# Optimization experiments

Hardware: AMD Instinct MI355X
Metric: run time of the kernel (lower is better)

Reference implementation:

```python
import math
import jax, jax.numpy as jnp
import numpy as np

N, L, H, E, K = 4, 768, 8, 64, 1  # batch, seq (L==S), heads, feat, num_sines


def setup_inputs() -> dict:
    key = jax.random.key(0)
    ks = jax.random.split(key, 8)
    queries = jax.random.normal(ks[0], (N, L, H, E), jnp.float32)
    keys = jax.random.normal(ks[1], (N, L, H, E), jnp.float32)
    values = jax.random.normal(ks[2], (N, L, H, E), jnp.float32)
    attn_mask_add = jnp.zeros((L, L), jnp.float32)
    key_lengths_add = jnp.zeros((N, L), jnp.float32)
    freqs = jax.random.normal(ks[3], (H, E, K), jnp.float32) - 4.0  # init shift
    offsets = jax.random.normal(ks[4], (H, E, K), jnp.float32)
    gains = jax.random.normal(ks[5], (H, E, K), jnp.float32)
    # gains.data /= sqrt(||gains||_{-1}) / 2
    gains = gains / (jnp.sqrt(jnp.linalg.norm(gains, axis=-1, keepdims=True)) / 2.0)
    gate = jax.random.normal(ks[6], (H, E), jnp.float32)
    return dict(queries=queries, keys=keys, values=values,
                attn_mask_add=attn_mask_add, key_lengths_add=key_lengths_add,
                freqs=freqs, offsets=offsets, gains=gains, gate=gate)


def reference(queries, keys, values, attn_mask_add, key_lengths_add,
              freqs, offsets, gains, gate):
    n, l, h, e = queries.shape
    softmax_temp = 1.0 / math.sqrt(e)
    positions = jnp.arange(l, dtype=queries.dtype)  # (L,)
    f = jax.nn.sigmoid(freqs)[None] / 2.0  # (1,H,E,K)
    phases_q = 2.0 * math.pi * f * positions[:, None, None, None] + offsets[None]
    phases_k = 2.0 * math.pi * f * positions[:, None, None, None]
    # interleave cos/sin along last dim -> (L,H,E,2K)
    omega_q = jnp.stack([jnp.cos(phases_q), jnp.sin(phases_q)], axis=-1).reshape(l, h, e, 2 * f.shape[-1])
    omega_k = jnp.stack([jnp.cos(phases_k), jnp.sin(phases_k)], axis=-1).reshape(l, h, e, 2 * f.shape[-1])
    g = jax.nn.softplus(gains)
    g2 = jnp.stack([g, g], axis=-1).reshape(h, e, 2 * f.shape[-1])  # (H,E,2K)
    # positional kernel P: (L,S,H,E)
    P = jnp.einsum('lhdk,hdk,shdk->lshd', omega_q, g2 ** 2, omega_k)
    P = (1.0 - gate) * P + gate  # gated
    QK = jnp.einsum('nlhd,lshd,nshd->nhls', queries, P, keys)
    QK = QK + attn_mask_add[None, None] + key_lengths_add[:, None, None, :]
    A = jax.nn.softmax(softmax_temp * QK, axis=-1)
    V = jnp.einsum('nhls,nshd->nlhd', A, values)
    return V
```

## Files before the change

kernel.cpp:

```cpp
#include <hip/hip_runtime.h>
#include <math.h>
#include <stdint.h>

#define NB 4
#define LQ 768
#define NH 8
#define NE 64
#define ND 192
#define TEMP 0.125f

typedef _Float16 f16;
typedef __attribute__((ext_vector_type(8))) _Float16 f16x8;
typedef __attribute__((ext_vector_type(4))) float f32x4;

__device__ __forceinline__ void stage16(f16* lds_base, const f16* g, int lane) {
#if __has_builtin(__builtin_amdgcn_global_load_lds)
    __builtin_amdgcn_global_load_lds(
        (const __attribute__((address_space(1))) uint32_t*)g,
        (__attribute__((address_space(3))) uint32_t*)lds_base, 16, 0, 0);
#else
    *(uint4*)((char*)lds_base + lane * 16) = *(const uint4*)g;
#endif
}

template <int CTRL>
__device__ __forceinline__ float dppf(float x) {
    union { float f; int i; } u, r;
    u.f = x;
    r.i = __builtin_amdgcn_update_dpp(u.i, u.i, CTRL, 0xF, 0xF, false);
    return r.f;
}
__device__ __forceinline__ float red16_max(float x) {
    x = fmaxf(x, dppf<0xB1>(x));
    x = fmaxf(x, dppf<0x4E>(x));
    x = fmaxf(x, dppf<0x141>(x));
    x = fmaxf(x, dppf<0x140>(x));
    return x;
}
__device__ __forceinline__ float red16_sum(float x) {
    x += dppf<0xB1>(x);
    x += dppf<0x4E>(x);
    x += dppf<0x141>(x);
    x += dppf<0x140>(x);
    return x;
}

__global__ __launch_bounds__(256) void sinattn_prep(
    const float* __restrict__ Q, const float* __restrict__ K,
    const float* __restrict__ freqs, const float* __restrict__ offsets,
    const float* __restrict__ gains, const float* __restrict__ gate,
    f16* __restrict__ Qf, f16* __restrict__ Kf)
{
    int idx = blockIdx.x * 256 + threadIdx.x;
    int eg = idx & 7, e0 = eg << 3;
    int h  = (idx >> 3) & 7;
    int t  = idx >> 6;
    int l  = t % LQ;
    int n  = t / LQ;
    int nh = (n << 3) | h;
    int he = (h << 6) | e0;

    const float* qp = Q + (size_t)idx * 8;
    const float* kp = K + (size_t)idx * 8;
    float4 q0 = *(const float4*)qp, q1 = *(const float4*)(qp + 4);
    float4 k0 = *(const float4*)kp, k1 = *(const float4*)(kp + 4);
    float qv[8] = {q0.x,q0.y,q0.z,q0.w, q1.x,q1.y,q1.z,q1.w};
    float kv[8] = {k0.x,k0.y,k0.z,k0.w, k1.x,k1.y,k1.z,k1.w};

    float4 fA = *(const float4*)(freqs   + he), fB = *(const float4*)(freqs   + he + 4);
    float4 oA = *(const float4*)(offsets + he), oB = *(const float4*)(offsets + he + 4);
    float4 gA = *(const float4*)(gains   + he), gB = *(const float4*)(gains   + he + 4);
    float4 tA = *(const float4*)(gate    + he), tB = *(const float4*)(gate    + he + 4);
    float fv[8] = {fA.x,fA.y,fA.z,fA.w, fB.x,fB.y,fB.z,fB.w};
    float ov[8] = {oA.x,oA.y,oA.z,oA.w, oB.x,oB.y,oB.z,oB.w};
    float gv[8] = {gA.x,gA.y,gA.z,gA.w, gB.x,gB.y,gB.z,gB.w};
    float tv[8] = {tA.x,tA.y,tA.z,tA.w, tB.x,tB.y,tB.z,tB.w};

    f16x8 oq0, oq1, oq2, ok0, ok1, ok2;
    float lf = (float)l;
    #pragma unroll
    for (int j = 0; j < 8; ++j) {
        float f  = 0.5f / (1.0f + __expf(-fv[j]));
        float gn = gv[j];
        float sp = (gn > 15.0f) ? gn : __logf(1.0f + __expf(gn));
        float gt = tv[j];
        float a  = (1.0f - gt) * sp * sp;
        float fh = __uint_as_float(__float_as_uint(f) & 0xFFFFF000u);
        float fl = f - fh;
        float t0 = lf * fh;
        float tr = t0 - floorf(t0);
        tr = __builtin_fmaf(lf, fl, tr);
        float pk = 6.28318530717958647f * tr;
        float pq = pk + ov[j];
        float sq = __sinf(pq), cq = __cosf(pq);
        float sk = __sinf(pk), ck = __cosf(pk);
        oq0[j] = (f16)(qv[j] * a * cq);
        oq1[j] = (f16)(qv[j] * a * sq);
        oq2[j] = (f16)(qv[j] * gt);
        ok0[j] = (f16)(kv[j] * ck);
        ok1[j] = (f16)(kv[j] * sk);
        ok2[j] = (f16)(kv[j]);
    }
    size_t base = ((size_t)nh * LQ + l) * ND + e0;
    *(f16x8*)(Qf + base)            = oq0;
    *(f16x8*)(Qf + base + NE)       = oq1;
    *(f16x8*)(Qf + base + 2 * NE)   = oq2;
    *(f16x8*)(Kf + base)            = ok0;
    *(f16x8*)(Kf + base + NE)       = ok1;
    *(f16x8*)(Kf + base + 2 * NE)   = ok2;
}

__global__ __launch_bounds__(256) void sinattn_vt(
    const float* __restrict__ V, f16* __restrict__ Vt)
{
    __shared__ f16 tile[64][72];
    int b = blockIdx.x;
    int st = b % 12, nh = b / 12;
    int n = nh >> 3, h = nh & 7;
    int s0 = st * 64;
    int tid = threadIdx.x;

    int sl = tid >> 2, e0 = (tid & 3) << 4;
    const float4* vp = (const float4*)(V + ((size_t)(n * LQ + s0 + sl) * NH + h) * NE + e0);
    float4 a0 = vp[0], a1 = vp[1], a2 = vp[2], a3 = vp[3];
    float vv[16] = { a0.x,a0.y,a0.z,a0.w, a1.x,a1.y,a1.z,a1.w,
                     a2.x,a2.y,a2.z,a2.w, a3.x,a3.y,a3.z,a3.w };
    #pragma unroll
    for (int j = 0; j < 16; ++j) tile[e0 + j][sl] = (f16)vv[j];
    __syncthreads();

    int er = tid >> 2, sc = tid & 3;
    f16* op = Vt + ((size_t)nh * NE + er) * LQ + s0 + sc * 16;
    *(uint4*)op       = *(const uint4*)&tile[er][sc * 16];
    *(uint4*)(op + 8) = *(const uint4*)&tile[er][sc * 16 + 8];
}

__global__ __launch_bounds__(128, 2) void sinattn_flash(
    const f16* __restrict__ Qf, const f16* __restrict__ Kf, const f16* __restrict__ Vt,
    const float* __restrict__ mask, const float* __restrict__ keylen,
    float* __restrict__ out)
{
    __shared__ __attribute__((aligned(16))) f16 sK[2][64 * 24 * 8];
    __shared__ __attribute__((aligned(16))) f16 sV[2][64 * 8 * 8];
    __shared__ __attribute__((aligned(16))) f16 sP[2][32 * 72];

    int tid  = threadIdx.x;
    int wv   = tid >> 6;
    int lane = tid & 63;
    int grp  = lane >> 4;
    int r16  = lane & 15;
    int swz  = r16 & 7;

    int bid = blockIdx.x;
    int nh  = bid & 31;
    int lt  = bid >> 5;
    int n   = nh >> 3;
    int l0  = lt * 64;

    f16x8 qf[2][6];
    #pragma unroll
    for (int ti = 0; ti < 2; ++ti) {
        size_t rbase = ((size_t)nh * LQ + l0 + wv * 32 + ti * 16 + r16) * ND + grp * 8;
        #pragma unroll
        for (int d0 = 0; d0 < 6; ++d0)
            qf[ti][d0] = *(const f16x8*)(Qf + rbase + d0 * 32);
    }

    int goffK[12], goffV[4];
    #pragma unroll
    for (int i = 0; i < 12; ++i) {
        int p = i * 128 + tid;
        int r = p / 24, c = p - r * 24;
        int cl = (c & ~7) | ((c & 7) ^ (r & 7));
        goffK[i] = r * ND + cl * 8;
    }
    #pragma unroll
    for (int i = 0; i < 4; ++i) {
        int p = i * 128 + tid;
        int r = p >> 3, c = p & 7;
        goffV[i] = r * LQ + (c ^ (r & 7)) * 8;
    }
    const f16* Kb = Kf + (size_t)nh * LQ * ND;
    const f16* Vb = Vt + (size_t)nh * NE * LQ;

    {
        #pragma unroll
        for (int i = 0; i < 12; ++i)
            stage16(&sK[0][(i * 128 + wv * 64) * 8], Kb + goffK[i], lane);
        #pragma unroll
        for (int i = 0; i < 4; ++i)
            stage16(&sV[0][(i * 128 + wv * 64) * 8], Vb + goffV[i], lane);
    }

    float m_i[2][4], l_i[2][4];
    f32x4 O[2][4];
    #pragma unroll
    for (int ti = 0; ti < 2; ++ti)
        #pragma unroll
        for (int rr = 0; rr < 4; ++rr) { m_i[ti][rr] = -INFINITY; l_i[ti][rr] = 0.f; }
    #pragma unroll
    for (int ti = 0; ti < 2; ++ti)
        #pragma unroll
        for (int tt = 0; tt < 4; ++tt)
            #pragma unroll
            for (int rr = 0; rr < 4; ++rr) O[ti][tt][rr] = 0.f;

    for (int c = 0; c < 12; ++c) {
        int cur = c & 1;
        int s0  = c * 64;
        __syncthreads();

        if (c < 11) {
            const f16* kg = Kb + (s0 + 64) * ND;
            const f16* vg = Vb + (s0 + 64);
            #pragma unroll
            for (int i = 0; i < 12; ++i)
                stage16(&sK[cur ^ 1][(i * 128 + wv * 64) * 8], kg + goffK[i], lane);
            #pragma unroll
            for (int i = 0; i < 4; ++i)
                stage16(&sV[cur ^ 1][(i * 128 + wv * 64) * 8], vg + goffV[i], lane);
        }

        float klv[4], mreg[2][4][4];
        #pragma unroll
        for (int j = 0; j < 4; ++j) klv[j] = keylen[n * LQ + s0 + j * 16 + r16];
        #pragma unroll
        for (int ti = 0; ti < 2; ++ti)
            #pragma unroll
            for (int rr = 0; rr < 4; ++rr) {
                int lrow = l0 + wv * 32 + ti * 16 + grp * 4 + rr;
                #pragma unroll
                for (int j = 0; j < 4; ++j)
                    mreg[ti][rr][j] = mask[lrow * LQ + s0 + j * 16 + r16];
            }

        f32x4 st[2][4];
        #pragma unroll
        for (int ti = 0; ti < 2; ++ti)
            #pragma unroll
            for (int j = 0; j < 4; ++j)
                #pragma unroll
                for (int rr = 0; rr < 4; ++rr) st[ti][j][rr] = 0.f;
        #pragma unroll
        for (int d0 = 0; d0 < 6; ++d0) {
            #pragma unroll
            for (int j = 0; j < 4; ++j) {
                int cc = d0 * 4 + grp;
                int cl = (cc & ~7) | ((cc & 7) ^ swz);
                f16x8 bf = *(const f16x8*)&sK[cur][((j * 16 + r16) * 24 + cl) * 8];
                st[0][j] = __builtin_amdgcn_mfma_f32_16x16x32_f16(qf[0][d0], bf, st[0][j], 0, 0, 0);
                st[1][j] = __builtin_amdgcn_mfma_f32_16x16x32_f16(qf[1][d0], bf, st[1][j], 0, 0, 0);
            }
        }

        #pragma unroll
        for (int ti = 0; ti < 2; ++ti) {
            #pragma unroll
            for (int rr = 0; rr < 4; ++rr) {
                float lg[4];
                float mx = -INFINITY;
                #pragma unroll
                for (int j = 0; j < 4; ++j) {
                    lg[j] = TEMP * (st[ti][j][rr] + mreg[ti][rr][j] + klv[j]);
                    mx = fmaxf(mx, lg[j]);
                }
                mx = red16_max(mx);
                float mnew  = fmaxf(m_i[ti][rr], mx);
                float alpha = __expf(m_i[ti][rr] - mnew);
                float rs = 0.f;
                #pragma unroll
                for (int j = 0; j < 4; ++j) {
                    float p = __expf(lg[j] - mnew);
                    rs += p;
                    sP[wv][(ti * 16 + grp * 4 + rr) * 72 + j * 16 + r16] = (f16)p;
                }
                rs = red16_sum(rs);
                l_i[ti][rr] = l_i[ti][rr] * alpha + rs;
                m_i[ti][rr] = mnew;
                #pragma unroll
                for (int tt = 0; tt < 4; ++tt) O[ti][tt][rr] *= alpha;
            }
        }

        #pragma unroll
        for (int kk = 0; kk < 2; ++kk) {
            f16x8 pa0 = *(const f16x8*)&sP[wv][(r16) * 72 + kk * 32 + grp * 8];
            f16x8 pa1 = *(const f16x8*)&sP[wv][(16 + r16) * 72 + kk * 32 + grp * 8];
            #pragma unroll
            for (int tt = 0; tt < 4; ++tt) {
                int cc = kk * 4 + grp;
                f16x8 vb = *(const f16x8*)&sV[cur][((tt * 16 + r16) * 8 + (cc ^ swz)) * 8];
                O[0][tt] = __builtin_amdgcn_mfma_f32_16x16x32_f16(pa0, vb, O[0][tt], 0, 0, 0);
                O[1][tt] = __builtin_amdgcn_mfma_f32_16x16x32_f16(pa1, vb, O[1][tt], 0, 0, 0);
            }
        }
    }

    #pragma unroll
    for (int ti = 0; ti < 2; ++ti) {
        #pragma unroll
        for (int rr = 0; rr < 4; ++rr) {
            float inv = 1.0f / l_i[ti][rr];
            int lrow = l0 + wv * 32 + ti * 16 + grp * 4 + rr;
            float* op = out + ((size_t)(n * LQ + lrow) * NH + (nh & 7)) * NE;
            #pragma unroll
            for (int tt = 0; tt < 4; ++tt)
                op[tt * 16 + r16] = O[ti][tt][rr] * inv;
        }
    }
}

extern "C" void kernel_launch(void* const* d_in, const int* in_sizes, int n_in,
                              void* d_out, int out_size, void* d_ws, size_t ws_size,
                              hipStream_t stream)
{
    const float* Q      = (const float*)d_in[0];
    const float* K      = (const float*)d_in[1];
    const float* V      = (const float*)d_in[2];
    const float* mask   = (const float*)d_in[3];
    const float* keylen = (const float*)d_in[4];
    const float* freqs  = (const float*)d_in[5];
    const float* offs   = (const float*)d_in[6];
    const float* gains  = (const float*)d_in[7];
    const float* gate   = (const float*)d_in[8];
    float* out = (float*)d_out;

    const size_t P = (size_t)NB * NH * LQ * ND;
    f16* Qf = (f16*)d_ws;
    f16* Kf = Qf + P;
    f16* Vt = Kf + P;

    sinattn_prep<<<768, 256, 0, stream>>>(Q, K, freqs, offs, gains, gate, Qf, Kf);
    sinattn_vt<<<384, 256, 0, stream>>>(V, Vt);
    sinattn_flash<<<NB * NH * (LQ / 64), 128, 0, stream>>>(Qf, Kf, Vt,
                                                           mask, keylen, out);
}
```

Before: 122.4 us.

## Merge V transpose into prep, use 3-wave 96-row blocks with 128-key chunks and exp2

The V-transpose kernel is folded into the prep kernel as extra blocks, which removes one launch. The flash kernel now uses 192 threads (3 waves) covering 96 query rows and stages 128-key chunks, so each K/V tile load is shared across more query rows and there are fewer barriers. The softmax switches to exp2 with log2e folded into the temperature, and s_setprio wraps the MFMA sections. The grid shrinks from 384 to 256 blocks and LDS use grows, which may lower occupancy or leave CUs underused.

After: 121.0 us. No clear change (-1.2%).

```diff
diff --git a/kernel.cpp b/kernel.cpp
--- a/kernel.cpp
+++ b/kernel.cpp
@@ -7,7 +7,7 @@
 #define NH 8
 #define NE 64
 #define ND 192
-#define TEMP 0.125f
+#define TEMP2 0.18033688011112042f
 
 typedef _Float16 f16;
 typedef __attribute__((ext_vector_type(8))) _Float16 f16x8;
@@ -23,6 +23,14 @@
 #endif
 }
 
+__device__ __forceinline__ float fexp2(float x) {
+#if __has_builtin(__builtin_amdgcn_exp2f)
+    return __builtin_amdgcn_exp2f(x);
+#else
+    return exp2f(x);
+#endif
+}
+
 template <int CTRL>
 __device__ __forceinline__ float dppf(float x) {
     union { float f; int i; } u, r;
@@ -47,11 +55,38 @@
 
 __global__ __launch_bounds__(256) void sinattn_prep(
     const float* __restrict__ Q, const float* __restrict__ K,
+    const float* __restrict__ V,
     const float* __restrict__ freqs, const float* __restrict__ offsets,
     const float* __restrict__ gains, const float* __restrict__ gate,
-    f16* __restrict__ Qf, f16* __restrict__ Kf)
+    f16* __restrict__ Qf, f16* __restrict__ Kf, f16* __restrict__ Vt)
 {
-    int idx = blockIdx.x * 256 + threadIdx.x;
+    __shared__ f16 tile[64][72];
+    int bid = blockIdx.x;
+    int tid = threadIdx.x;
+
+    if (bid >= 768) {
+        int b = bid - 768;
+        int st = b % 12, nh = b / 12;
+        int n = nh >> 3, h = nh & 7;
+        int s0 = st * 64;
+
+        int sl = tid >> 2, e0 = (tid & 3) << 4;
+        const float4* vp = (const float4*)(V + ((size_t)(n * LQ + s0 + sl) * NH + h) * NE + e0);
+        float4 a0 = vp[0], a1 = vp[1], a2 = vp[2], a3 = vp[3];
+        float vv[16] = { a0.x,a0.y,a0.z,a0.w, a1.x,a1.y,a1.z,a1.w,
+                         a2.x,a2.y,a2.z,a2.w, a3.x,a3.y,a3.z,a3.w };
+        #pragma unroll
+        for (int j = 0; j < 16; ++j) tile[e0 + j][sl] = (f16)vv[j];
+        __syncthreads();
+
+        int er = tid >> 2, sc = tid & 3;
+        f16* op = Vt + ((size_t)nh * NE + er) * LQ + s0 + sc * 16;
+        *(uint4*)op       = *(const uint4*)&tile[er][sc * 16];
+        *(uint4*)(op + 8) = *(const uint4*)&tile[er][sc * 16 + 8];
+        return;
+    }
+
+    int idx = bid * 256 + tid;
     int eg = idx & 7, e0 = eg << 3;
     int h  = (idx >> 3) & 7;
     int t  = idx >> 6;
@@ -110,42 +145,17 @@
     *(f16x8*)(Kf + base + 2 * NE)   = ok2;
 }
 
-__global__ __launch_bounds__(256) void sinattn_vt(
-    const float* __restrict__ V, f16* __restrict__ Vt)
-{
-    __shared__ f16 tile[64][72];
-    int b = blockIdx.x;
-    int st = b % 12, nh = b / 12;
-    int n = nh >> 3, h = nh & 7;
-    int s0 = st * 64;
-    int tid = threadIdx.x;
-
-    int sl = tid >> 2, e0 = (tid & 3) << 4;
-    const float4* vp = (const float4*)(V + ((size_t)(n * LQ + s0 + sl) * NH + h) * NE + e0);
-    float4 a0 = vp[0], a1 = vp[1], a2 = vp[2], a3 = vp[3];
-    float vv[16] = { a0.x,a0.y,a0.z,a0.w, a1.x,a1.y,a1.z,a1.w,
-                     a2.x,a2.y,a2.z,a2.w, a3.x,a3.y,a3.z,a3.w };
-    #pragma unroll
-    for (int j = 0; j < 16; ++j) tile[e0 + j][sl] = (f16)vv[j];
-    __syncthreads();
-
-    int er = tid >> 2, sc = tid & 3;
-    f16* op = Vt + ((size_t)nh * NE + er) * LQ + s0 + sc * 16;
-    *(uint4*)op       = *(const uint4*)&tile[er][sc * 16];
-    *(uint4*)(op + 8) = *(const uint4*)&tile[er][sc * 16 + 8];
-}
-
-__global__ __launch_bounds__(128, 2) void sinattn_flash(
+__global__ __launch_bounds__(192) void sinattn_flash(
     const f16* __restrict__ Qf, const f16* __restrict__ Kf, const f16* __restrict__ Vt,
     const float* __restrict__ mask, const float* __restrict__ keylen,
     float* __restrict__ out)
 {
-    __shared__ __attribute__((aligned(16))) f16 sK[2][64 * 24 * 8];
-    __shared__ __attribute__((aligned(16))) f16 sV[2][64 * 8 * 8];
-    __shared__ __attribute__((aligned(16))) f16 sP[2][32 * 72];
+    __shared__ __attribute__((aligned(16))) f16 sK[2][128 * 24 * 8];
+    __shared__ __attribute__((aligned(16))) f16 sV[2][64 * 16 * 8];
+    __shared__ __attribute__((aligned(16))) f16 sP[3][32 * 72];
 
     int tid  = threadIdx.x;
-    int wv   = tid >> 6;
+    int wv   = tid / 64;
     int lane = tid & 63;
     int grp  = lane >> 4;
     int r16  = lane & 15;
@@ -155,41 +165,45 @@
     int nh  = bid & 31;
     int lt  = bid >> 5;
     int n   = nh >> 3;
-    int l0  = lt * 64;
-
-    f16x8 qf[2][6];
-    #pragma unroll
-    for (int ti = 0; ti < 2; ++ti) {
-        size_t rbase = ((size_t)nh * LQ + l0 + wv * 32 + ti * 16 + r16) * ND + grp * 8;
-        #pragma unroll
-        for (int d0 = 0; d0 < 6; ++d0)
-            qf[ti][d0] = *(const f16x8*)(Qf + rbase + d0 * 32);
-    }
-
-    int goffK[12], goffV[4];
-    #pragma unroll
-    for (int i = 0; i < 12; ++i) {
-        int p = i * 128 + tid;
+    int l0  = lt * 96;
+    int qrow0 = l0 + wv * 32;
+
+    int goffK[16], goffV[6];
+    #pragma unroll
+    for (int i = 0; i < 16; ++i) {
+        int p = i * 192 + tid;
         int r = p / 24, c = p - r * 24;
         int cl = (c & ~7) | ((c & 7) ^ (r & 7));
         goffK[i] = r * ND + cl * 8;
     }
     #pragma unroll
-    for (int i = 0; i < 4; ++i) {
-        int p = i * 128 + tid;
-        int r = p >> 3, c = p & 7;
-        goffV[i] = r * LQ + (c ^ (r & 7)) * 8;
+    for (int i = 0; i < 6; ++i) {
+        int p = i * 192 + tid;
+        int r = p >> 4, c = p & 15;
+        int cl = (c & ~7) | ((c & 7) ^ (r & 7));
+        goffV[i] = r * LQ + cl * 8;
     }
     const f16* Kb = Kf + (size_t)nh * LQ * ND;
     const f16* Vb = Vt + (size_t)nh * NE * LQ;
 
     {
         #pragma unroll
-        for (int i = 0; i < 12; ++i)
-            stage16(&sK[0][(i * 128 + wv * 64) * 8], Kb + goffK[i], lane);
-        #pragma unroll
-        for (int i = 0; i < 4; ++i)
-            stage16(&sV[0][(i * 128 + wv * 64) * 8], Vb + goffV[i], lane);
+        for (int i = 0; i < 16; ++i)
+            stage16(&sK[0][(i * 192 + wv * 64) * 8], Kb + goffK[i], lane);
+        #pragma unroll
+        for (int i = 0; i < 5; ++i)
+            stage16(&sV[0][(i * 192 + wv * 64) * 8], Vb + goffV[i], lane);
+        if (tid < 64)
+            stage16(&sV[0][(960 + wv * 64) * 8], Vb + goffV[5], lane);
+    }
+
+    f16x8 qf[2][6];
+    #pragma unroll
+    for (int ti = 0; ti < 2; ++ti) {
+        size_t rbase = ((size_t)nh * LQ + qrow0 + ti * 16 + r16) * ND + grp * 8;
+        #pragma unroll
+        for (int d0 = 0; d0 < 6; ++d0)
+            qf[ti][d0] = *(const f16x8*)(Qf + rbase + d0 * 32);
     }
 
     float m_i[2][4], l_i[2][4];
@@ -205,94 +219,108 @@
             #pragma unroll
             for (int rr = 0; rr < 4; ++rr) O[ti][tt][rr] = 0.f;
 
-    for (int c = 0; c < 12; ++c) {
+    for (int c = 0; c < 6; ++c) {
         int cur = c & 1;
-        int s0  = c * 64;
+        int cs0 = c * 128;
         __syncthreads();
 
-        if (c < 11) {
-            const f16* kg = Kb + (s0 + 64) * ND;
-            const f16* vg = Vb + (s0 + 64);
-            #pragma unroll
-            for (int i = 0; i < 12; ++i)
-                stage16(&sK[cur ^ 1][(i * 128 + wv * 64) * 8], kg + goffK[i], lane);
-            #pragma unroll
-            for (int i = 0; i < 4; ++i)
-                stage16(&sV[cur ^ 1][(i * 128 + wv * 64) * 8], vg + goffV[i], lane);
+        if (c < 5) {
+            const f16* kg = Kb + (cs0 + 128) * ND;
+            const f16* vg = Vb + (cs0 + 128);
+            #pragma unroll
+            for (int i = 0; i < 16; ++i)
+                stage16(&sK[cur ^ 1][(i * 192 + wv * 64) * 8], kg + goffK[i], lane);
+            #pragma unroll
+            for (int i = 0; i < 5; ++i)
+                stage16(&sV[cur ^ 1][(i * 192 + wv * 64) * 8], vg + goffV[i], lane);
+            if (tid < 64)
+                stage16(&sV[cur ^ 1][(960 + wv * 64) * 8], vg + goffV[5], lane);
         }
 
-        float klv[4], mreg[2][4][4];
-        #pragma unroll
-        for (int j = 0; j < 4; ++j) klv[j] = keylen[n * LQ + s0 + j * 16 + r16];
-        #pragma unroll
-        for (int ti = 0; ti < 2; ++ti)
-            #pragma unroll
-            for (int rr = 0; rr < 4; ++rr) {
-                int lrow = l0 + wv * 32 + ti * 16 + grp * 4 + rr;
+        #pragma unroll
+        for (int pp = 0; pp < 2; ++pp) {
+            int s0 = cs0 + pp * 64;
+
+            float klv[4], mreg[2][4][4];
+            #pragma unroll
+            for (int j = 0; j < 4; ++j) klv[j] = keylen[n * LQ + s0 + j * 16 + r16];
+            #pragma unroll
+            for (int ti = 0; ti < 2; ++ti)
+                #pragma unroll
+                for (int rr = 0; rr < 4; ++rr) {
+                    int lrow = qrow0 + ti * 16 + grp * 4 + rr;
+                    #pragma unroll
+                    for (int j = 0; j < 4; ++j)
+                        mreg[ti][rr][j] = mask[lrow * LQ + s0 + j * 16 + r16];
+                }
+
+            f32x4 st[2][4];
+            #pragma unroll
+            for (int ti = 0; ti < 2; ++ti)
                 #pragma unroll
                 for (int j = 0; j < 4; ++j)
-                    mreg[ti][rr][j] = mask[lrow * LQ + s0 + j * 16 + r16];
+                    #pragma unroll
+                    for (int rr = 0; rr < 4; ++rr) st[ti][j][rr] = 0.f;
+            __builtin_amdgcn_s_setprio(1);
+            #pragma unroll
+            for (int d0 = 0; d0 < 6; ++d0) {
+                #pragma unroll
+                for (int j = 0; j < 4; ++j) {
+                    int kr = pp * 64 + j * 16 + r16;
+                    int cc = d0 * 4 + grp;
+                    int cl = (cc & ~7) | ((cc & 7) ^ ((kr & 7)));
+                    f16x8 bf = *(const f16x8*)&sK[cur][(kr * 24 + cl) * 8];
+                    st[0][j] = __builtin_amdgcn_mfma_f32_16x16x32_f16(qf[0][d0], bf, st[0][j], 0, 0, 0);
+                    st[1][j] = __builtin_amdgcn_mfma_f32_16x16x32_f16(qf[1][d0], bf, st[1][j], 0, 0, 0);
+                }
             }
-
-        f32x4 st[2][4];
-        #pragma unroll
-        for (int ti = 0; ti < 2; ++ti)
-            #pragma unroll
-            for (int j = 0; j < 4; ++j)
-                #pragma unroll
-                for (int rr = 0; rr < 4; ++rr) st[ti][j][rr] = 0.f;
-        #pragma unroll
-        for (int d0 = 0; d0 < 6; ++d0) {
-            #pragma unroll
-            for (int j = 0; j < 4; ++j) {
-                int cc = d0 * 4 + grp;
-                int cl = (cc & ~7) | ((cc & 7) ^ swz);
-                f16x8 bf = *(const f16x8*)&sK[cur][((j * 16 + r16) * 24 + cl) * 8];
-                st[0][j] = __builtin_amdgcn_mfma_f32_16x16x32_f16(qf[0][d0], bf, st[0][j], 0, 0, 0);
-                st[1][j] = __builtin_amdgcn_mfma_f32_16x16x32_f16(qf[1][d0], bf, st[1][j], 0, 0, 0);
+            __builtin_amdgcn_s_setprio(0);
+
+            #pragma unroll
+            for (int ti = 0; ti < 2; ++ti) {
+                #pragma unroll
+                for (int rr = 0; rr < 4; ++rr) {
+                    float lg[4];
+                    float mx = -INFINITY;
+                    #pragma unroll
+                    for (int j = 0; j < 4; ++j) {
+                        lg[j] = TEMP2 * (st[ti][j][rr] + mreg[ti][rr][j] + klv[j]);
+                        mx = fmaxf(mx, lg[j]);
+                    }
+                    mx = red16_max(mx);
+                    float mnew  = fmaxf(m_i[ti][rr], mx);
+                    float alpha = fexp2(m_i[ti][rr] - mnew);
+                    float rs = 0.f;
+                    #pragma unroll
+                    for (int j = 0; j < 4; ++j) {
+                        float p = fexp2(lg[j] - mnew);
+                        rs += p;
+                        sP[wv][(ti * 16 + grp * 4 + rr) * 72 + j * 16 + r16] = (f16)p;
+                    }
+                    rs = red16_sum(rs);
+                    l_i[ti][rr] = l_i[ti][rr] * alpha + rs;
+                    m_i[ti][rr] = mnew;
+                    #pragma unroll
+                    for (int tt = 0; tt < 4; ++tt) O[ti][tt][rr] *= alpha;
+                }
             }
-        }
-
-        #pragma unroll
-        for (int ti = 0; ti < 2; ++ti) {
-            #pragma unroll
-            for (int rr = 0; rr < 4; ++rr) {
-                float lg[4];
-                float mx = -INFINITY;
-                #pragma unroll
-                for (int j = 0; j < 4; ++j) {
-                    lg[j] = TEMP * (st[ti][j][rr] + mreg[ti][rr][j] + klv[j]);
-                    mx = fmaxf(mx, lg[j]);
+
+            __builtin_amdgcn_s_setprio(1);
+            #pragma unroll
+            for (int kk = 0; kk < 2; ++kk) {
+                f16x8 pa0 = *(const f16x8*)&sP[wv][(r16) * 72 + kk * 32 + grp * 8];
+                f16x8 pa1 = *(const f16x8*)&sP[wv][(16 + r16) * 72 + kk * 32 + grp * 8];
+                #pragma unroll
+                for (int tt = 0; tt < 4; ++tt) {
+                    int er = tt * 16 + r16;
+                    int cc = pp * 8 + kk * 4 + grp;
+                    int cl = (cc & ~7) | ((cc & 7) ^ (er & 7));
+                    f16x8 vb = *(const f16x8*)&sV[cur][(er * 16 + cl) * 8];
+                    O[0][tt] = __builtin_amdgcn_mfma_f32_16x16x32_f16(pa0, vb, O[0][tt], 0, 0, 0);
+                    O[1][tt] = __builtin_amdgcn_mfma_f32_16x16x32_f16(pa1, vb, O[1][tt], 0, 0, 0);
                 }
-                mx = red16_max(mx);
-                float mnew  = fmaxf(m_i[ti][rr], mx);
-                float alpha = __expf(m_i[ti][rr] - mnew);
-                float rs = 0.f;
-                #pragma unroll
-                for (int j = 0; j < 4; ++j) {
-                    float p = __expf(lg[j] - mnew);
-                    rs += p;
-                    sP[wv][(ti * 16 + grp * 4 + rr) * 72 + j * 16 + r16] = (f16)p;
-                }
-                rs = red16_sum(rs);
-                l_i[ti][rr] = l_i[ti][rr] * alpha + rs;
-                m_i[ti][rr] = mnew;
-                #pragma unroll
-                for (int tt = 0; tt < 4; ++tt) O[ti][tt][rr] *= alpha;
             }
-        }
-
-        #pragma unroll
-        for (int kk = 0; kk < 2; ++kk) {
-            f16x8 pa0 = *(const f16x8*)&sP[wv][(r16) * 72 + kk * 32 + grp * 8];
-            f16x8 pa1 = *(const f16x8*)&sP[wv][(16 + r16) * 72 + kk * 32 + grp * 8];
-            #pragma unroll
-            for (int tt = 0; tt < 4; ++tt) {
-                int cc = kk * 4 + grp;
-                f16x8 vb = *(const f16x8*)&sV[cur][((tt * 16 + r16) * 8 + (cc ^ swz)) * 8];
-                O[0][tt] = __builtin_amdgcn_mfma_f32_16x16x32_f16(pa0, vb, O[0][tt], 0, 0, 0);
-                O[1][tt] = __builtin_amdgcn_mfma_f32_16x16x32_f16(pa1, vb, O[1][tt], 0, 0, 0);
-            }
+            __builtin_amdgcn_s_setprio(0);
         }
     }
 
@@ -301,7 +329,7 @@
         #pragma unroll
         for (int rr = 0; rr < 4; ++rr) {
             float inv = 1.0f / l_i[ti][rr];
-            int lrow = l0 + wv * 32 + ti * 16 + grp * 4 + rr;
+            int lrow = qrow0 + ti * 16 + grp * 4 + rr;
             float* op = out + ((size_t)(n * LQ + lrow) * NH + (nh & 7)) * NE;
             #pragma unroll
             for (int tt = 0; tt < 4; ++tt)
@@ -330,8 +358,8 @@
     f16* Kf = Qf + P;
     f16* Vt = Kf + P;
 
-    sinattn_prep<<<768, 256, 0, stream>>>(Q, K, freqs, offs, gains, gate, Qf, Kf);
-    sinattn_vt<<<384, 256, 0, stream>>>(V, Vt);
-    sinattn_flash<<<NB * NH * (LQ / 64), 128, 0, stream>>>(Qf, Kf, Vt,
+    sinattn_prep<<<768 + 384, 256, 0, stream>>>(Q, K, V, freqs, offs, gains, gate,
+                                                Qf, Kf, Vt);
+    sinattn_flash<<<NB * NH * (LQ / 96), 192, 0, stream>>>(Qf, Kf, Vt,
                                                            mask, keylen, out);
 }
```
